# Kernel tuning notes

Measured on AMD Instinct MI355X. Metric: run time of the kernel, lower is better.

The kernel has to match this reference:

```python
import jax, jax.numpy as jnp
import numpy as np


def setup_inputs() -> dict:
    key = jax.random.key(0)
    ks = jax.random.split(key, 8)
    B, Te, De, Dd, H = 64, 1024, 1024, 1024, 1024
    return {
        "encoder_outputs": jax.random.normal(ks[0], (B, Te, De), jnp.float32),
        "decoder_outputs": jax.random.normal(ks[1], (B, 1, Dd), jnp.float32),
        "Wa_w": jax.random.normal(ks[2], (H, Dd), jnp.float32) * 0.02,
        "Wa_b": jax.random.normal(ks[3], (H,), jnp.float32) * 0.02,
        "Ua_w": jax.random.normal(ks[4], (H, De), jnp.float32) * 0.02,
        "Ua_b": jax.random.normal(ks[5], (H,), jnp.float32) * 0.02,
        "Va_w": jax.random.normal(ks[6], (1, H), jnp.float32) * 0.02,
        "Va_b": jax.random.normal(ks[7], (1,), jnp.float32) * 0.02,
    }


def reference(encoder_outputs, decoder_outputs, Wa_w, Wa_b, Ua_w, Ua_b, Va_w, Va_b):
    # Wa: [B,1,H], Ua: [B,Te,H]  (torch Linear: x @ W.T + b)
    Wa = jnp.einsum('bqd,hd->bqh', decoder_outputs, Wa_w) + Wa_b
    Ua = jnp.einsum('bed,hd->beh', encoder_outputs, Ua_w) + Ua_b
    # broadcast add -> tanh -> scalar score per encoder position: [B,Te,1]
    scores = jnp.einsum('beh,oh->beo', jnp.tanh(Wa + Ua), Va_w) + Va_b
    scores = jnp.transpose(scores, (0, 2, 1))          # [B,1,Te]
    weights = jax.nn.softmax(scores, axis=-1)          # softmax over Te
    context = jnp.einsum('bqe,bed->bqd', weights, encoder_outputs)  # [B,1,De]
    return context
```

## Files before the change

kernel.cpp:

```cpp
#include <hip/hip_runtime.h>
#include <hip/hip_bf16.h>

#define B_  64
#define TE  1024
#define K_  1024
#define HH  1024
#define MM  (B_ * TE)

typedef __bf16 bf16x8 __attribute__((ext_vector_type(8)));
typedef __bf16 bf16x4 __attribute__((ext_vector_type(4)));
typedef float  f32x4  __attribute__((ext_vector_type(4)));

__device__ __forceinline__ float fast_tanh(float x) {
    float ax = __builtin_fabsf(x);
    float t  = __expf(-2.0f * ax);
    float r  = (1.0f - t) * __builtin_amdgcn_rcpf(1.0f + t);
    return __builtin_copysignf(r, x);
}

__global__ void cvt_kernel(const float* __restrict__ in, __bf16* __restrict__ out, long n4) {
    long i = (long)blockIdx.x * blockDim.x + threadIdx.x;
    long stride = (long)gridDim.x * blockDim.x;
    const float4* in4 = (const float4*)in;
    bf16x4* out4 = (bf16x4*)out;
    for (long j = i; j < n4; j += stride) {
        float4 v = in4[j];
        bf16x4 o;
        o[0] = (__bf16)v.x; o[1] = (__bf16)v.y; o[2] = (__bf16)v.z; o[3] = (__bf16)v.w;
        out4[j] = o;
    }
}

__global__ void wa_kernel(const float* __restrict__ dec, const float* __restrict__ Wa_w,
                          const float* __restrict__ Wa_b, float* __restrict__ WaOut) {
    int b = blockIdx.x, ht = blockIdx.y;
    int wave = threadIdx.x >> 6, lane = threadIdx.x & 63;
    const float* db = dec + b * 1024;
    for (int i = 0; i < 16; i++) {
        int h = ht * 64 + wave * 16 + i;
        const float* wr = Wa_w + (long)h * 1024;
        float a = 0.0f;
        #pragma unroll
        for (int k = 0; k < 16; k++)
            a += db[lane + 64 * k] * wr[lane + 64 * k];
        #pragma unroll
        for (int off = 32; off > 0; off >>= 1)
            a += __shfl_xor(a, off, 64);
        if (lane == 0) WaOut[b * 1024 + h] = a + Wa_b[h];
    }
}

#define MT 128
#define NP 256
#define KT 64

__global__ __launch_bounds__(256, 2) void score_gemm(
    const float* __restrict__ Af,
    __bf16* __restrict__ encB,
    const __bf16* __restrict__ Bm,
    const float* __restrict__ Wa,
    const float* __restrict__ Ua_b,
    const float* __restrict__ Va_w,
    float* __restrict__ scores)
{
    __shared__ __bf16 sA[MT * KT];
    __shared__ __bf16 sB[NP * KT];
    __shared__ float sVa[NP];
    __shared__ float sWU[NP];

    const int tid  = threadIdx.x;
    const int wave = tid >> 6;
    const int lane = tid & 63;
    const int quad = lane >> 4;
    const int l16  = lane & 15;
    const int wm   = wave >> 1;
    const int wn   = wave & 1;

    const int bid = blockIdx.x;
    const int grp = bid >> 5;
    const int r5  = bid & 31;
    const int y   = r5 >> 3;
    const int x   = grp * 8 + (r5 & 7);

    const int rowBase = x * MT;
    const int colBase = y * NP;
    const int b       = rowBase >> 10;
    const bool wb     = (y == 0);

    if (tid < NP) {
        int h = colBase + tid;
        sVa[tid] = Va_w[h];
        sWU[tid] = Wa[b * 1024 + h] + Ua_b[h];
    }

    int rr[4], sg[4];
    #pragma unroll
    for (int i = 0; i < 4; i++) {
        int c = i * 256 + tid;
        rr[i] = c >> 3;
        sg[i] = (c & 7) ^ (rr[i] & 7);
    }

    f32x4 acc[4][8] = {};

    const long aBase = (long)rowBase * K_;
    const long bBase = (long)colBase * K_;

    float4 pre[4][2];
    #pragma unroll
    for (int i = 0; i < 4; i++) {
        const float4* p = (const float4*)(Af + aBase + (long)rr[i] * K_ + sg[i] * 8);
        pre[i][0] = p[0]; pre[i][1] = p[1];
    }

    for (int k0 = 0; k0 < K_; k0 += KT) {
        __syncthreads();
        #pragma unroll
        for (int i = 0; i < 4; i++) {
            bf16x8 v;
            v[0] = (__bf16)pre[i][0].x; v[1] = (__bf16)pre[i][0].y;
            v[2] = (__bf16)pre[i][0].z; v[3] = (__bf16)pre[i][0].w;
            v[4] = (__bf16)pre[i][1].x; v[5] = (__bf16)pre[i][1].y;
            v[6] = (__bf16)pre[i][1].z; v[7] = (__bf16)pre[i][1].w;
            *(bf16x8*)(sA + (i * 256 + tid) * 8) = v;
            if (wb)
                *(bf16x8*)(encB + aBase + (long)rr[i] * K_ + k0 + sg[i] * 8) = v;
        }
        #pragma unroll
        for (int i = 0; i < 8; i++) {
            int c = i * 256 + tid;
            int r = c >> 3, slot = c & 7;
            int seg = slot ^ (r & 7);
            __builtin_amdgcn_global_load_lds(
                (const __attribute__((address_space(1))) unsigned int*)(Bm + bBase + (long)r * K_ + k0 + seg * 8),
                (__attribute__((address_space(3))) unsigned int*)(sB + c * 8), 16, 0, 0);
        }
        __syncthreads();

        if (k0 + KT < K_) {
            #pragma unroll
            for (int i = 0; i < 4; i++) {
                const float4* p = (const float4*)(Af + aBase + (long)rr[i] * K_ + (k0 + KT) + sg[i] * 8);
                pre[i][0] = p[0]; pre[i][1] = p[1];
            }
        }

        #pragma unroll
        for (int ks = 0; ks < 2; ks++) {
            bf16x8 bfr[8];
            #pragma unroll
            for (int t = 0; t < 8; t++) {
                int r = wn * 128 + t * 16 + l16;
                int slot = (ks * 4 + quad) ^ (r & 7);
                bfr[t] = *(const bf16x8*)(sB + r * KT + slot * 8);
            }
            #pragma unroll
            for (int s = 0; s < 4; s++) {
                int r = wm * 64 + s * 16 + l16;
                int slot = (ks * 4 + quad) ^ (r & 7);
                bf16x8 af = *(const bf16x8*)(sA + r * KT + slot * 8);
                #pragma unroll
                for (int t = 0; t < 8; t++)
                    acc[s][t] = __builtin_amdgcn_mfma_f32_16x16x32_bf16(af, bfr[t], acc[s][t], 0, 0, 0);
            }
        }
    }

    float rs[4][4] = {};
    #pragma unroll
    for (int s = 0; s < 4; s++)
        #pragma unroll
        for (int t = 0; t < 8; t++) {
            int hl = wn * 128 + t * 16 + l16;
            float va = sVa[hl], wu = sWU[hl];
            #pragma unroll
            for (int r = 0; r < 4; r++)
                rs[s][r] += va * fast_tanh(acc[s][t][r] + wu);
        }

    #pragma unroll
    for (int s = 0; s < 4; s++)
        #pragma unroll
        for (int r = 0; r < 4; r++) {
            float v = rs[s][r];
            v += __shfl_xor(v, 1, 64);
            v += __shfl_xor(v, 2, 64);
            v += __shfl_xor(v, 4, 64);
            v += __shfl_xor(v, 8, 64);
            if (l16 == 0)
                atomicAdd(&scores[rowBase + wm * 64 + s * 16 + quad * 4 + r], v);
        }
}

__global__ void softmax_kernel(float* __restrict__ s) {
    __shared__ float red[256];
    int b = blockIdx.x, tid = threadIdx.x;
    float4* row = (float4*)(s + b * 1024);
    float4 v = row[tid];
    float m = fmaxf(fmaxf(v.x, v.y), fmaxf(v.z, v.w));
    red[tid] = m; __syncthreads();
    for (int off = 128; off > 0; off >>= 1) {
        if (tid < off) red[tid] = fmaxf(red[tid], red[tid + off]);
        __syncthreads();
    }
    m = red[0]; __syncthreads();
    v.x = expf(v.x - m); v.y = expf(v.y - m); v.z = expf(v.z - m); v.w = expf(v.w - m);
    red[tid] = v.x + v.y + v.z + v.w; __syncthreads();
    for (int off = 128; off > 0; off >>= 1) {
        if (tid < off) red[tid] += red[tid + off];
        __syncthreads();
    }
    float inv = 1.0f / red[0];
    v.x *= inv; v.y *= inv; v.z *= inv; v.w *= inv;
    row[tid] = v;
}

__global__ void context_kernel(const __bf16* __restrict__ enc, const float* __restrict__ w,
                               float* __restrict__ out) {
    int b = blockIdx.x, ec = blockIdx.y, tid = threadIdx.x;
    const bf16x4* enc4 = (const bf16x4*)(enc + ((long)b * 1024 + ec * 64) * 1024);
    const float* wrow = w + b * 1024 + ec * 64;
    float ax = 0, ay = 0, az = 0, aw = 0;
    for (int e = 0; e < 64; e++) {
        float we = wrow[e];
        bf16x4 v = enc4[e * 256 + tid];
        ax += we * (float)v[0]; ay += we * (float)v[1];
        az += we * (float)v[2]; aw += we * (float)v[3];
    }
    float* o = out + b * 1024 + tid * 4;
    atomicAdd(o + 0, ax); atomicAdd(o + 1, ay);
    atomicAdd(o + 2, az); atomicAdd(o + 3, aw);
}

extern "C" void kernel_launch(void* const* d_in, const int* in_sizes, int n_in,
                              void* d_out, int out_size, void* d_ws, size_t ws_size,
                              hipStream_t stream) {
    (void)in_sizes; (void)n_in; (void)ws_size;
    const float* enc   = (const float*)d_in[0];
    const float* dec   = (const float*)d_in[1];
    const float* Wa_w  = (const float*)d_in[2];
    const float* Wa_b  = (const float*)d_in[3];
    const float* Ua_w  = (const float*)d_in[4];
    const float* Ua_b  = (const float*)d_in[5];
    const float* Va_w  = (const float*)d_in[6];
    float* out = (float*)d_out;

    char* w = (char*)d_ws;
    __bf16* encB = (__bf16*)w;  w += (size_t)MM * 1024 * 2;
    __bf16* uawB = (__bf16*)w;  w += (size_t)HH * 1024 * 2;
    float* WaBuf = (float*)w;   w += (size_t)B_ * HH * 4;
    float* scores = (float*)w;  w += (size_t)MM * 4;

    hipMemsetAsync(scores, 0, (size_t)MM * 4, stream);
    hipMemsetAsync(out, 0, (size_t)out_size * 4, stream);
    cvt_kernel<<<dim3(256), 256, 0, stream>>>(Ua_w, uawB, (long)HH * 1024 / 4);
    wa_kernel<<<dim3(B_, 16), 256, 0, stream>>>(dec, Wa_w, Wa_b, WaBuf);
    score_gemm<<<dim3((MM / MT) * (HH / NP)), 256, 0, stream>>>(enc, encB, uawB, WaBuf, Ua_b, Va_w, scores);
    softmax_kernel<<<dim3(B_), 256, 0, stream>>>(scores);
    context_kernel<<<dim3(B_, 16), 256, 0, stream>>>(encB, scores, out);
}
```

Before: 528.2 us.

## Vectorize Wa and context kernels, raise score GEMM occupancy, issue B loads earlier

The Wa projection kernel now keeps the decoder row in registers and reads the weights as float4, changing which k each lane sums over. The score GEMM's launch bounds go from 2 to 3 blocks per SIMD, and the async global-to-LDS loads for the B tile are issued before the A-tile convert and store so they overlap with that work. The context kernel reads bf16x8 vectors, with two groups of threads splitting the encoder positions. The higher occupancy target may force register spills in the GEMM, which holds a large accumulator array.

```diff
diff --git a/kernel.cpp b/kernel.cpp
--- a/kernel.cpp
+++ b/kernel.cpp
@@ -31,18 +31,28 @@
     }
 }
 
-__global__ void wa_kernel(const float* __restrict__ dec, const float* __restrict__ Wa_w,
-                          const float* __restrict__ Wa_b, float* __restrict__ WaOut) {
-    int b = blockIdx.x, ht = blockIdx.y;
+__global__ __launch_bounds__(256) void wa_kernel(const float* __restrict__ dec,
+                                                 const float* __restrict__ Wa_w,
+                                                 const float* __restrict__ Wa_b,
+                                                 float* __restrict__ WaOut) {
+    int b = blockIdx.x, hc = blockIdx.y;
     int wave = threadIdx.x >> 6, lane = threadIdx.x & 63;
-    const float* db = dec + b * 1024;
+
+    const float4* d4 = (const float4*)(dec + b * 1024);
+    float4 dreg[4];
+    #pragma unroll
+    for (int j = 0; j < 4; j++) dreg[j] = d4[lane * 4 + j];
+
+    #pragma unroll 4
     for (int i = 0; i < 16; i++) {
-        int h = ht * 64 + wave * 16 + i;
-        const float* wr = Wa_w + (long)h * 1024;
+        int h = hc * 64 + wave * 16 + i;
+        const float4* wr = (const float4*)(Wa_w + (long)h * 1024);
         float a = 0.0f;
         #pragma unroll
-        for (int k = 0; k < 16; k++)
-            a += db[lane + 64 * k] * wr[lane + 64 * k];
+        for (int j = 0; j < 4; j++) {
+            float4 v = wr[lane * 4 + j];
+            a += v.x * dreg[j].x + v.y * dreg[j].y + v.z * dreg[j].z + v.w * dreg[j].w;
+        }
         #pragma unroll
         for (int off = 32; off > 0; off >>= 1)
             a += __shfl_xor(a, off, 64);
@@ -54,7 +64,7 @@
 #define NP 256
 #define KT 64
 
-__global__ __launch_bounds__(256, 2) void score_gemm(
+__global__ __launch_bounds__(256, 3) void score_gemm(
     const float* __restrict__ Af,
     __bf16* __restrict__ encB,
     const __bf16* __restrict__ Bm,
@@ -116,6 +126,15 @@
     for (int k0 = 0; k0 < K_; k0 += KT) {
         __syncthreads();
         #pragma unroll
+        for (int i = 0; i < 8; i++) {
+            int c = i * 256 + tid;
+            int r = c >> 3, slot = c & 7;
+            int seg = slot ^ (r & 7);
+            __builtin_amdgcn_global_load_lds(
+                (const __attribute__((address_space(1))) unsigned int*)(Bm + bBase + (long)r * K_ + k0 + seg * 8),
+                (__attribute__((address_space(3))) unsigned int*)(sB + c * 8), 16, 0, 0);
+        }
+        #pragma unroll
         for (int i = 0; i < 4; i++) {
             bf16x8 v;
             v[0] = (__bf16)pre[i][0].x; v[1] = (__bf16)pre[i][0].y;
@@ -126,15 +145,6 @@
             if (wb)
                 *(bf16x8*)(encB + aBase + (long)rr[i] * K_ + k0 + sg[i] * 8) = v;
         }
-        #pragma unroll
-        for (int i = 0; i < 8; i++) {
-            int c = i * 256 + tid;
-            int r = c >> 3, slot = c & 7;
-            int seg = slot ^ (r & 7);
-            __builtin_amdgcn_global_load_lds(
-                (const __attribute__((address_space(1))) unsigned int*)(Bm + bBase + (long)r * K_ + k0 + seg * 8),
-                (__attribute__((address_space(3))) unsigned int*)(sB + c * 8), 16, 0, 0);
-        }
         __syncthreads();
 
         if (k0 + KT < K_) {
@@ -215,21 +225,25 @@
     row[tid] = v;
 }
 
-__global__ void context_kernel(const __bf16* __restrict__ enc, const float* __restrict__ w,
-                               float* __restrict__ out) {
+__global__ __launch_bounds__(256) void context_kernel(const __bf16* __restrict__ enc,
+                                                      const float* __restrict__ w,
+                                                      float* __restrict__ out) {
     int b = blockIdx.x, ec = blockIdx.y, tid = threadIdx.x;
-    const bf16x4* enc4 = (const bf16x4*)(enc + ((long)b * 1024 + ec * 64) * 1024);
+    int eo = tid >> 7;
+    int dc = tid & 127;
+    const bf16x8* enc8 = (const bf16x8*)(enc + ((long)b * 1024 + ec * 64) * 1024);
     const float* wrow = w + b * 1024 + ec * 64;
-    float ax = 0, ay = 0, az = 0, aw = 0;
-    for (int e = 0; e < 64; e++) {
+    float acc[8] = {};
+    #pragma unroll 4
+    for (int e = eo; e < 64; e += 2) {
         float we = wrow[e];
-        bf16x4 v = enc4[e * 256 + tid];
-        ax += we * (float)v[0]; ay += we * (float)v[1];
-        az += we * (float)v[2]; aw += we * (float)v[3];
-    }
-    float* o = out + b * 1024 + tid * 4;
-    atomicAdd(o + 0, ax); atomicAdd(o + 1, ay);
-    atomicAdd(o + 2, az); atomicAdd(o + 3, aw);
+        bf16x8 v = enc8[e * 128 + dc];
+        #pragma unroll
+        for (int j = 0; j < 8; j++) acc[j] += we * (float)v[j];
+    }
+    float* o = out + b * 1024 + dc * 8;
+    #pragma unroll
+    for (int j = 0; j < 8; j++) atomicAdd(o + j, acc[j]);
 }
 
 extern "C" void kernel_launch(void* const* d_in, const int* in_sizes, int n_in,
```

Result: slower. 1.384 ms (+162.1%).
